# Kernel tuning notes

Hardware: AMD Instinct MI355X
Metric: run time of the kernel (lower is better)

## Reference

```python
import jax, jax.numpy as jnp
import numpy as np
import math

B, S, D = 4, 2048, 768
H = 12
DH = D // H  # 64
NEG = -1e10

def setup_inputs() -> dict:
    key = jax.random.key(0)
    ks = jax.random.split(key, 8)
    scale = 0.02
    return {
        "hidden_states": jax.random.normal(ks[0], (B, S, D), dtype=jnp.float32),
        "attention_mask": jnp.zeros((B, 1, 1, S), dtype=jnp.float32),
        "Wq": jax.random.normal(ks[1], (D, D), dtype=jnp.float32) * scale,
        "bq": jnp.zeros((D,), dtype=jnp.float32),
        "Wk": jax.random.normal(ks[2], (D, D), dtype=jnp.float32) * scale,
        "bk": jnp.zeros((D,), dtype=jnp.float32),
        "Wv": jax.random.normal(ks[3], (D, D), dtype=jnp.float32) * scale,
        "bv": jnp.zeros((D,), dtype=jnp.float32),
    }

def reference(hidden_states, attention_mask, Wq, bq, Wk, bk, Wv, bv):
    # Linear projections; note attention_mask is accepted but unused, matching the torch module.
    def split_heads(x):  # [B,S,D] -> [B,H,S,DH]
        return x.reshape(B, S, H, DH).transpose(0, 2, 1, 3)
    q = split_heads(hidden_states @ Wq + bq)
    k = split_heads(hidden_states @ Wk + bk)
    v = split_heads(hidden_states @ Wv + bv)
    scores = jnp.einsum("bhqd,bhkd->bhqk", q, k) / math.sqrt(DH)
    causal = jnp.tril(jnp.ones((S, S), dtype=bool))  # masked_fill(mask==0, -1e10)
    scores = jnp.where(causal, scores, NEG)
    probs = jax.nn.softmax(scores, axis=-1)
    # dropout prob = 0.0 (eval) -> identity
    ctx = jnp.einsum("bhqk,bhkd->bhqd", probs, v)
    return ctx.transpose(0, 2, 1, 3).reshape(B, S, D)
```

## Files before the change

kernel.cpp:

```cpp
#include <hip/hip_runtime.h>
#include <hip/hip_bf16.h>

#define B_  4
#define S_  2048
#define D_  768
#define H_  12
#define DH_ 64

#define QSCALE 0.1803368802f

typedef __bf16 bf16;
typedef __attribute__((ext_vector_type(8))) __bf16 bf16x8;
typedef __attribute__((ext_vector_type(4))) __bf16 bf16x4;
typedef __attribute__((ext_vector_type(4))) float floatx4;
typedef __attribute__((ext_vector_type(4))) short short4v;

#if defined(__has_builtin)
#if __has_builtin(__builtin_amdgcn_mfma_f32_16x16x16bf16_1k)
#define HAVE_MFMA16_BUILTIN 1
#endif
#endif
static __device__ __forceinline__ floatx4 mfma16(short4v a, short4v b, floatx4 c) {
#ifdef HAVE_MFMA16_BUILTIN
    return __builtin_amdgcn_mfma_f32_16x16x16bf16_1k(a, b, c, 0, 0, 0);
#else
    floatx4 d = c;
    asm("v_mfma_f32_16x16x16_bf16 %0, %1, %2, %0" : "+v"(d) : "v"(a), "v"(b));
    return d;
#endif
}

__device__ __forceinline__ int swz(int row, int col) {
    return row * 64 + (col ^ ((row & 7) << 3));
}

__device__ __forceinline__ void gload16(const bf16* g, bf16* l) {
    __builtin_amdgcn_global_load_lds(
        (const __attribute__((address_space(1))) void*)g,
        (__attribute__((address_space(3))) void*)l, 16, 0, 0);
}

__device__ __forceinline__ int chunk_off(int qt) {
    if (qt < 8)  return qt;
    if (qt < 16) return 8 + 2 * (qt - 8);
    if (qt < 24) return 24 + 3 * (qt - 16);
    return 48 + 4 * (qt - 24);
}

__global__ __launch_bounds__(256) void prep(const float* __restrict__ hs,
                                            const float* __restrict__ w0,
                                            const float* __restrict__ w1,
                                            const float* __restrict__ w2,
                                            bf16* __restrict__ Xb,
                                            bf16* __restrict__ Wt)
{
    __shared__ bf16 t[64 * 72];
    const int bid = blockIdx.x;
    const int tid = threadIdx.x;
    if (bid < 6144) {
        int i = bid * 256 + tid;
        float4 v = ((const float4*)hs)[i];
        bf16x4 o;
        o[0] = (bf16)v.x; o[1] = (bf16)v.y; o[2] = (bf16)v.z; o[3] = (bf16)v.w;
        *(bf16x4*)(Xb + (size_t)i * 4) = o;
        return;
    }
    const int t4 = bid - 6144;
    const int which = t4 / 144;
    const int rem = t4 % 144;
    const float* W = (which == 0) ? w0 : (which == 1 ? w1 : w2);
    const float sc = (which == 0) ? QSCALE : 1.0f;
    bf16* dst = Wt + (size_t)which * D_ * D_;
    const int k0 = (rem / 12) * 64, n0 = (rem % 12) * 64;
    {
        int r = tid >> 2;
        int c0 = (tid & 3) * 16;
        #pragma unroll
        for (int q = 0; q < 4; q++) {
            float4 v = *(const float4*)(W + (size_t)(k0 + r) * D_ + n0 + c0 + q * 4);
            t[(c0 + q * 4 + 0) * 72 + r] = (bf16)(v.x * sc);
            t[(c0 + q * 4 + 1) * 72 + r] = (bf16)(v.y * sc);
            t[(c0 + q * 4 + 2) * 72 + r] = (bf16)(v.z * sc);
            t[(c0 + q * 4 + 3) * 72 + r] = (bf16)(v.w * sc);
        }
    }
    __syncthreads();
    {
        int n = tid >> 3, seg = tid & 7;
        *(bf16x8*)(dst + (size_t)(n0 + n) * D_ + k0 + seg * 8) =
            *(const bf16x8*)(t + n * 72 + seg * 8);
        *(bf16x8*)(dst + (size_t)(n0 + n + 32) * D_ + k0 + seg * 8) =
            *(const bf16x8*)(t + (n + 32) * 72 + seg * 8);
    }
}

__global__ __launch_bounds__(256) void qkv_gemm(
    const bf16* __restrict__ Xb, const bf16* __restrict__ Wt,
    const float* __restrict__ bq, const float* __restrict__ bk,
    const float* __restrict__ bv, bf16* __restrict__ QKV)
{
    const int which = blockIdx.z;
    const bf16* Wm = Wt + (size_t)which * D_ * D_;
    const float* bias = (which == 0) ? bq : (which == 1 ? bk : bv);
    const float bscale = (which == 0) ? QSCALE : 1.0f;
    bf16* out = QKV + (size_t)which * B_ * H_ * S_ * DH_;

    __shared__ bf16 As[128 * 64];
    __shared__ bf16 Bs[128 * 64];

    const int tid  = threadIdx.x;
    const int wave = tid >> 6, lane = tid & 63;
    const int wr = wave >> 1, wc = wave & 1;
    const int g = lane >> 4, ln = lane & 15;
    const int m0 = blockIdx.x * 128, n0 = blockIdx.y * 128;

    floatx4 acc[4][4];
    #pragma unroll
    for (int i = 0; i < 4; i++)
        #pragma unroll
        for (int j = 0; j < 4; j++)
            acc[i][j] = (floatx4){0.f, 0.f, 0.f, 0.f};

    int row_[4], scol_[4];
    #pragma unroll
    for (int t = 0; t < 4; t++) {
        int c = tid + t * 256;
        row_[t]  = c >> 3;
        scol_[t] = ((c & 7) * 8) ^ ((row_[t] & 7) << 3);
    }

    for (int k0 = 0; k0 < D_; k0 += 64) {
        if (k0) __syncthreads();
        #pragma unroll
        for (int t = 0; t < 4; t++) {
            bf16* ldst = As + (size_t)(t * 256 + wave * 64) * 8;
            gload16(Xb + (size_t)(m0 + row_[t]) * D_ + k0 + scol_[t], ldst);
        }
        #pragma unroll
        for (int t = 0; t < 4; t++) {
            bf16* ldst = Bs + (size_t)(t * 256 + wave * 64) * 8;
            gload16(Wm + (size_t)(n0 + row_[t]) * D_ + k0 + scol_[t], ldst);
        }
        __syncthreads();
        #pragma unroll
        for (int ks = 0; ks < 2; ks++) {
            bf16x8 af[4], bfr[4];
            #pragma unroll
            for (int i = 0; i < 4; i++)
                af[i] = *(const bf16x8*)(As + swz(wr * 64 + i * 16 + ln, ks * 32 + g * 8));
            #pragma unroll
            for (int j = 0; j < 4; j++)
                bfr[j] = *(const bf16x8*)(Bs + swz(wc * 64 + j * 16 + ln, ks * 32 + g * 8));
            if (which == 2) {
                #pragma unroll
                for (int i = 0; i < 4; i++)
                    #pragma unroll
                    for (int j = 0; j < 4; j++)
                        acc[i][j] = __builtin_amdgcn_mfma_f32_16x16x32_bf16(af[i], bfr[j], acc[i][j], 0, 0, 0);
            } else {
                #pragma unroll
                for (int i = 0; i < 4; i++)
                    #pragma unroll
                    for (int j = 0; j < 4; j++)
                        acc[i][j] = __builtin_amdgcn_mfma_f32_16x16x32_bf16(bfr[j], af[i], acc[i][j], 0, 0, 0);
            }
        }
    }

    if (which == 2) {
        #pragma unroll
        for (int i = 0; i < 4; i++) {
            #pragma unroll
            for (int j = 0; j < 4; j++) {
                int col = n0 + wc * 64 + j * 16 + ln;
                float bv_ = bias[col];
                int h = col >> 6, dh = col & 63;
                int rowbase = m0 + wr * 64 + i * 16 + g * 4;
                int b = rowbase >> 11, s0 = rowbase & 2047;
                bf16x4 o;
                #pragma unroll
                for (int r = 0; r < 4; r++) o[r] = (bf16)(acc[i][j][r] + bv_);
                *(bf16x4*)(out + ((size_t)((b * H_ + h) * DH_ + dh)) * S_ + s0) = o;
            }
        }
    } else {
        #pragma unroll
        for (int i = 0; i < 4; i++) {
            int s = m0 + wr * 64 + i * 16 + ln;
            int b = s >> 11, s0 = s & 2047;
            #pragma unroll
            for (int j = 0; j < 4; j++) {
                int nb = n0 + wc * 64 + j * 16 + g * 4;
                int h = nb >> 6, dh0 = nb & 63;
                float4 bv4 = *(const float4*)(bias + nb);
                bf16x4 o;
                o[0] = (bf16)(acc[i][j][0] + bv4.x * bscale);
                o[1] = (bf16)(acc[i][j][1] + bv4.y * bscale);
                o[2] = (bf16)(acc[i][j][2] + bv4.z * bscale);
                o[3] = (bf16)(acc[i][j][3] + bv4.w * bscale);
                *(bf16x4*)(out + (((size_t)(b * H_ + h) * S_ + s0) << 6) + dh0) = o;
            }
        }
    }
}

__global__ __launch_bounds__(256, 4) void attn_chunk(const bf16* __restrict__ QKV,
                                                     float* __restrict__ out,
                                                     bf16* __restrict__ Opart,
                                                     float* __restrict__ Lpart)
{
    const int cid = 79 - blockIdx.x;
    const int bh = blockIdx.y;
    const int b = bh / H_, h = bh % H_;

    int qt, c;
    if (cid < 8)       { qt = cid; c = 0; }
    else if (cid < 24) { qt = 8 + ((cid - 8) >> 1); c = (cid - 8) & 1; }
    else if (cid < 48) { int t3 = cid - 24; qt = 16 + t3 / 3; c = t3 - (qt - 16) * 3; }
    else               { int t4 = cid - 48; qt = 24 + (t4 >> 2); c = t4 & 3; }
    const int nch = (qt >> 3) + 1;
    const int kt0 = c * 8;
    const int kt1 = min(kt0 + 7, qt);

    const size_t MAT = (size_t)B_ * H_ * S_ * DH_;
    const bf16* Q  = QKV +           (size_t)bh * S_ * DH_;
    const bf16* K  = QKV + MAT +     (size_t)bh * S_ * DH_;
    const bf16* Vt = QKV + 2 * MAT + (size_t)bh * S_ * DH_;

    __shared__ bf16 Ks[64 * 64];
    __shared__ bf16 Vts[64 * 64];

    const int tid  = threadIdx.x;
    const int wave = tid >> 6, lane = tid & 63;
    const int g = lane >> 4, ln = lane & 15;
    const int srow = tid >> 3, sseg = tid & 7;

    bf16x8 qf[2];
    {
        const bf16* qrow = Q + (size_t)(qt * 64 + wave * 16 + ln) * DH_;
        qf[0] = *(const bf16x8*)(qrow + g * 8);
        qf[1] = *(const bf16x8*)(qrow + 32 + g * 8);
    }

    const short4v ones16 = {0x3F80, 0x3F80, 0x3F80, 0x3F80};

    floatx4 accO[4];
    #pragma unroll
    for (int dt = 0; dt < 4; dt++) accO[dt] = (floatx4){0.f, 0.f, 0.f, 0.f};
    floatx4 accL = (floatx4){0.f, 0.f, 0.f, 0.f};

    const bf16* kptr = K  + (size_t)(kt0 * 64 + srow) * DH_ + sseg * 8;
    const bf16* vptr = Vt + (size_t)srow * S_ + kt0 * 64 + sseg * 8;

    bf16x8 ka = *(const bf16x8*)kptr;
    bf16x8 kb = *(const bf16x8*)(kptr + 32 * DH_);
    bf16x8 va = *(const bf16x8*)vptr;
    bf16x8 vb = *(const bf16x8*)(vptr + (size_t)32 * S_);

    for (int kt = kt0; kt <= kt1; ++kt) {
        __syncthreads();
        *(bf16x8*)(Ks  + swz(srow, sseg * 8)) = ka;
        *(bf16x8*)(Ks  + swz(srow + 32, sseg * 8)) = kb;
        *(bf16x8*)(Vts + swz(srow, sseg * 8)) = va;
        *(bf16x8*)(Vts + swz(srow + 32, sseg * 8)) = vb;
        __syncthreads();
        if (kt < kt1) {
            kptr += 64 * DH_;
            vptr += 64;
            ka = *(const bf16x8*)kptr;
            kb = *(const bf16x8*)(kptr + 32 * DH_);
            va = *(const bf16x8*)vptr;
            vb = *(const bf16x8*)(vptr + (size_t)32 * S_);
        }

        __builtin_amdgcn_s_setprio(1);
        #pragma unroll
        for (int j = 0; j < 4; j++) {
            floatx4 accS = (floatx4){0.f, 0.f, 0.f, 0.f};
            #pragma unroll
            for (int cc = 0; cc < 2; cc++) {
                bf16x8 kf = *(const bf16x8*)(Ks + swz(j * 16 + ln, cc * 32 + g * 8));
                accS = __builtin_amdgcn_mfma_f32_16x16x32_bf16(kf, qf[cc], accS, 0, 0, 0);
            }

            #pragma unroll
            for (int r = 0; r < 4; r++) accS[r] = __builtin_amdgcn_exp2f(accS[r]);
            if (kt == qt) {
                const int krow = j * 16 + g * 4;
                const int qrow = wave * 16 + ln;
                #pragma unroll
                for (int r = 0; r < 4; r++)
                    if (krow + r > qrow) accS[r] = 0.f;
            }

            bf16x4 pa;
            #pragma unroll
            for (int r = 0; r < 4; r++) pa[r] = (bf16)accS[r];
            short4v pas = __builtin_bit_cast(short4v, pa);

            accL = mfma16(pas, ones16, accL);

            #pragma unroll
            for (int dt = 0; dt < 4; dt++) {
                short4v vf = *(const short4v*)(Vts + swz(dt * 16 + ln, j * 16 + g * 4));
                accO[dt] = mfma16(pas, vf, accO[dt]);
            }
        }
        __builtin_amdgcn_s_setprio(0);
    }

    if (nch == 1) {
        float inv[4];
        #pragma unroll
        for (int r = 0; r < 4; r++) inv[r] = 1.0f / accL[r];
        #pragma unroll
        for (int dt = 0; dt < 4; dt++) {
            int dh = dt * 16 + ln;
            #pragma unroll
            for (int r = 0; r < 4; r++) {
                int q = qt * 64 + wave * 16 + g * 4 + r;
                out[((size_t)(b * S_ + q)) * D_ + h * DH_ + dh] = accO[dt][r] * inv[r];
            }
        }
    } else {
        const int chunk = bh * 80 + chunk_off(qt) + c;
        bf16x8 p0, p1;
        #pragma unroll
        for (int e = 0; e < 8; e++) {
            p0[e] = (bf16)accO[e >> 2][e & 3];
            p1[e] = (bf16)accO[2 + (e >> 2)][e & 3];
        }
        bf16* dst = Opart + (size_t)chunk * 4096 + tid * 16;
        *(bf16x8*)dst = p0;
        *(bf16x8*)(dst + 8) = p1;
        if (ln == 0) {
            #pragma unroll
            for (int r = 0; r < 4; r++)
                Lpart[chunk * 64 + wave * 16 + g * 4 + r] = accL[r];
        }
    }
}

__global__ __launch_bounds__(256) void attn_reduce(const bf16* __restrict__ Opart,
                                                   const float* __restrict__ Lpart,
                                                   float* __restrict__ out)
{
    const int qt = 8 + blockIdx.x;
    const int bh = blockIdx.y;
    const int b = bh / H_, h = bh % H_;
    const int nch = (qt >> 3) + 1;
    const int cb = bh * 80 + chunk_off(qt);

    const int tid  = threadIdx.x;
    const int wave = tid >> 6, lane = tid & 63;
    const int g = lane >> 4, ln = lane & 15;

    float o[16];
    #pragma unroll
    for (int e = 0; e < 16; e++) o[e] = 0.f;
    float ls[4] = {0.f, 0.f, 0.f, 0.f};

    for (int cidx = 0; cidx < nch; cidx++) {
        const bf16* p = Opart + (size_t)(cb + cidx) * 4096 + tid * 16;
        bf16x8 v0 = *(const bf16x8*)p;
        bf16x8 v1 = *(const bf16x8*)(p + 8);
        #pragma unroll
        for (int e = 0; e < 8; e++) { o[e] += (float)v0[e]; o[8 + e] += (float)v1[e]; }
        #pragma unroll
        for (int r = 0; r < 4; r++)
            ls[r] += Lpart[(cb + cidx) * 64 + wave * 16 + g * 4 + r];
    }
    float inv[4];
    #pragma unroll
    for (int r = 0; r < 4; r++) inv[r] = 1.0f / ls[r];
    #pragma unroll
    for (int j = 0; j < 4; j++) {
        int dh = j * 16 + ln;
        #pragma unroll
        for (int r = 0; r < 4; r++) {
            int q = qt * 64 + wave * 16 + g * 4 + r;
            out[((size_t)(b * S_ + q)) * D_ + h * DH_ + dh] = o[j * 4 + r] * inv[r];
        }
    }
}

extern "C" void kernel_launch(void* const* d_in, const int* in_sizes, int n_in,
                              void* d_out, int out_size, void* d_ws, size_t ws_size,
                              hipStream_t stream) {
    const float* hs = (const float*)d_in[0];
    const float* Wq = (const float*)d_in[2];
    const float* bq = (const float*)d_in[3];
    const float* Wk = (const float*)d_in[4];
    const float* bk = (const float*)d_in[5];
    const float* Wv = (const float*)d_in[6];
    const float* bv = (const float*)d_in[7];
    float* out = (float*)d_out;

    bf16* Xb    = (bf16*)d_ws;
    bf16* Wt    = Xb + (size_t)8192 * 768;
    bf16* QKV   = Wt + (size_t)3 * 768 * 768;
    bf16* Opart = QKV + (size_t)3 * B_ * H_ * S_ * DH_;
    float* Lpart = (float*)(Opart + (size_t)3840 * 4096);

    prep<<<6576, 256, 0, stream>>>(hs, Wq, Wk, Wv, Xb, Wt);
    qkv_gemm<<<dim3(64, 6, 3), 256, 0, stream>>>(Xb, Wt, bq, bk, bv, QKV);
    attn_chunk<<<dim3(80, 48), 256, 0, stream>>>(QKV, out, Opart, Lpart);
    attn_reduce<<<dim3(24, 48), 256, 0, stream>>>(Opart, Lpart, out);
}
```

Measured before the change: 220.4 us.

## Process two query tiles per attention block to reuse K/V tiles

Each attention_chunk block now handles two adjacent 64-row query tiles (128 queries), so every K/V tile staged in shared memory feeds twice as many MFMAs. The grid halves from 80 to 40 chunks per head, and the partial-output and row-sum buffers are relaid out to hold both tiles per chunk. The V-projection epilogue is also unified with the Q/K path: operand order is swapped and the transposed V is written as scalar strided stores. The cost is higher register pressure from the doubled accumulators, fewer blocks for load balancing, and less coalesced writes for V.

```diff
diff --git a/kernel.cpp b/kernel.cpp
--- a/kernel.cpp
+++ b/kernel.cpp
@@ -40,11 +40,11 @@
         (__attribute__((address_space(3))) void*)l, 16, 0, 0);
 }
 
-__device__ __forceinline__ int chunk_off(int qt) {
-    if (qt < 8)  return qt;
-    if (qt < 16) return 8 + 2 * (qt - 8);
-    if (qt < 24) return 24 + 3 * (qt - 16);
-    return 48 + 4 * (qt - 24);
+__device__ __forceinline__ int chunk_off(int qb) {
+    if (qb < 4)  return qb;
+    if (qb < 8)  return 4 + 2 * (qb - 4);
+    if (qb < 12) return 12 + 3 * (qb - 8);
+    return 24 + 4 * (qb - 12);
 }
 
 __global__ __launch_bounds__(256) void prep(const float* __restrict__ hs,
@@ -132,15 +132,13 @@
     for (int k0 = 0; k0 < D_; k0 += 64) {
         if (k0) __syncthreads();
         #pragma unroll
-        for (int t = 0; t < 4; t++) {
-            bf16* ldst = As + (size_t)(t * 256 + wave * 64) * 8;
-            gload16(Xb + (size_t)(m0 + row_[t]) * D_ + k0 + scol_[t], ldst);
-        }
-        #pragma unroll
-        for (int t = 0; t < 4; t++) {
-            bf16* ldst = Bs + (size_t)(t * 256 + wave * 64) * 8;
-            gload16(Wm + (size_t)(n0 + row_[t]) * D_ + k0 + scol_[t], ldst);
-        }
+        for (int t = 0; t < 4; t++)
+            gload16(Xb + (size_t)(m0 + row_[t]) * D_ + k0 + scol_[t],
+                    As + (size_t)(t * 256 + wave * 64) * 8);
+        #pragma unroll
+        for (int t = 0; t < 4; t++)
+            gload16(Wm + (size_t)(n0 + row_[t]) * D_ + k0 + scol_[t],
+                    Bs + (size_t)(t * 256 + wave * 64) * 8);
         __syncthreads();
         #pragma unroll
         for (int ks = 0; ks < 2; ks++) {
@@ -151,39 +149,15 @@
             #pragma unroll
             for (int j = 0; j < 4; j++)
                 bfr[j] = *(const bf16x8*)(Bs + swz(wc * 64 + j * 16 + ln, ks * 32 + g * 8));
-            if (which == 2) {
+            #pragma unroll
+            for (int i = 0; i < 4; i++)
                 #pragma unroll
-                for (int i = 0; i < 4; i++)
-                    #pragma unroll
-                    for (int j = 0; j < 4; j++)
-                        acc[i][j] = __builtin_amdgcn_mfma_f32_16x16x32_bf16(af[i], bfr[j], acc[i][j], 0, 0, 0);
-            } else {
-                #pragma unroll
-                for (int i = 0; i < 4; i++)
-                    #pragma unroll
-                    for (int j = 0; j < 4; j++)
-                        acc[i][j] = __builtin_amdgcn_mfma_f32_16x16x32_bf16(bfr[j], af[i], acc[i][j], 0, 0, 0);
-            }
-        }
-    }
-
-    if (which == 2) {
-        #pragma unroll
-        for (int i = 0; i < 4; i++) {
-            #pragma unroll
-            for (int j = 0; j < 4; j++) {
-                int col = n0 + wc * 64 + j * 16 + ln;
-                float bv_ = bias[col];
-                int h = col >> 6, dh = col & 63;
-                int rowbase = m0 + wr * 64 + i * 16 + g * 4;
-                int b = rowbase >> 11, s0 = rowbase & 2047;
-                bf16x4 o;
-                #pragma unroll
-                for (int r = 0; r < 4; r++) o[r] = (bf16)(acc[i][j][r] + bv_);
-                *(bf16x4*)(out + ((size_t)((b * H_ + h) * DH_ + dh)) * S_ + s0) = o;
-            }
-        }
-    } else {
+                for (int j = 0; j < 4; j++)
+                    acc[i][j] = __builtin_amdgcn_mfma_f32_16x16x32_bf16(bfr[j], af[i], acc[i][j], 0, 0, 0);
+        }
+    }
+
+    if (which < 2) {
         #pragma unroll
         for (int i = 0; i < 4; i++) {
             int s = m0 + wr * 64 + i * 16 + ln;
@@ -201,6 +175,23 @@
                 *(bf16x4*)(out + (((size_t)(b * H_ + h) * S_ + s0) << 6) + dh0) = o;
             }
         }
+    } else {
+        #pragma unroll
+        for (int i = 0; i < 4; i++) {
+            int s = m0 + wr * 64 + i * 16 + ln;
+            int b = s >> 11, s0 = s & 2047;
+            #pragma unroll
+            for (int j = 0; j < 4; j++) {
+                int nb = n0 + wc * 64 + j * 16 + g * 4;
+                int h = nb >> 6, dh0 = nb & 63;
+                float4 bv4 = *(const float4*)(bias + nb);
+                bf16* base = out + ((size_t)(b * H_ + h) * DH_ + dh0) * S_ + s0;
+                base[0]          = (bf16)(acc[i][j][0] + bv4.x);
+                base[S_]         = (bf16)(acc[i][j][1] + bv4.y);
+                base[2 * S_]     = (bf16)(acc[i][j][2] + bv4.z);
+                base[3 * (size_t)S_] = (bf16)(acc[i][j][3] + bv4.w);
+            }
+        }
     }
 }
 
@@ -209,18 +200,19 @@
                                                      bf16* __restrict__ Opart,
                                                      float* __restrict__ Lpart)
 {
-    const int cid = 79 - blockIdx.x;
+    const int cid = 39 - blockIdx.x;
     const int bh = blockIdx.y;
     const int b = bh / H_, h = bh % H_;
 
-    int qt, c;
-    if (cid < 8)       { qt = cid; c = 0; }
-    else if (cid < 24) { qt = 8 + ((cid - 8) >> 1); c = (cid - 8) & 1; }
-    else if (cid < 48) { int t3 = cid - 24; qt = 16 + t3 / 3; c = t3 - (qt - 16) * 3; }
-    else               { int t4 = cid - 48; qt = 24 + (t4 >> 2); c = t4 & 3; }
-    const int nch = (qt >> 3) + 1;
+    int qb, c;
+    if (cid < 4)       { qb = cid; c = 0; }
+    else if (cid < 12) { qb = 4 + ((cid - 4) >> 1); c = (cid - 4) & 1; }
+    else if (cid < 24) { int t = cid - 12; qb = 8 + t / 3; c = t - (qb - 8) * 3; }
+    else               { int t = cid - 24; qb = 12 + (t >> 2); c = t & 3; }
+    const int nch = (qb >> 2) + 1;
+    const int qt0 = 2 * qb, qt1 = 2 * qb + 1;
     const int kt0 = c * 8;
-    const int kt1 = min(kt0 + 7, qt);
+    const int kt1 = min(kt0 + 7, qt1);
 
     const size_t MAT = (size_t)B_ * H_ * S_ * DH_;
     const bf16* Q  = QKV +           (size_t)bh * S_ * DH_;
@@ -235,19 +227,26 @@
     const int g = lane >> 4, ln = lane & 15;
     const int srow = tid >> 3, sseg = tid & 7;
 
-    bf16x8 qf[2];
+    bf16x8 qf0[2], qf1[2];
     {
-        const bf16* qrow = Q + (size_t)(qt * 64 + wave * 16 + ln) * DH_;
-        qf[0] = *(const bf16x8*)(qrow + g * 8);
-        qf[1] = *(const bf16x8*)(qrow + 32 + g * 8);
+        const bf16* qrow = Q + (size_t)(qt0 * 64 + wave * 16 + ln) * DH_;
+        qf0[0] = *(const bf16x8*)(qrow + g * 8);
+        qf0[1] = *(const bf16x8*)(qrow + 32 + g * 8);
+        qrow += (size_t)64 * DH_;
+        qf1[0] = *(const bf16x8*)(qrow + g * 8);
+        qf1[1] = *(const bf16x8*)(qrow + 32 + g * 8);
     }
 
     const short4v ones16 = {0x3F80, 0x3F80, 0x3F80, 0x3F80};
 
-    floatx4 accO[4];
-    #pragma unroll
-    for (int dt = 0; dt < 4; dt++) accO[dt] = (floatx4){0.f, 0.f, 0.f, 0.f};
-    floatx4 accL = (floatx4){0.f, 0.f, 0.f, 0.f};
+    floatx4 accO0[4], accO1[4];
+    #pragma unroll
+    for (int dt = 0; dt < 4; dt++) {
+        accO0[dt] = (floatx4){0.f, 0.f, 0.f, 0.f};
+        accO1[dt] = (floatx4){0.f, 0.f, 0.f, 0.f};
+    }
+    floatx4 accL0 = (floatx4){0.f, 0.f, 0.f, 0.f};
+    floatx4 accL1 = (floatx4){0.f, 0.f, 0.f, 0.f};
 
     const bf16* kptr = K  + (size_t)(kt0 * 64 + srow) * DH_ + sseg * 8;
     const bf16* vptr = Vt + (size_t)srow * S_ + kt0 * 64 + sseg * 8;
@@ -273,70 +272,98 @@
             vb = *(const bf16x8*)(vptr + (size_t)32 * S_);
         }
 
+        const bool do0 = (kt <= qt0);
+
         __builtin_amdgcn_s_setprio(1);
         #pragma unroll
         for (int j = 0; j < 4; j++) {
-            floatx4 accS = (floatx4){0.f, 0.f, 0.f, 0.f};
-            #pragma unroll
-            for (int cc = 0; cc < 2; cc++) {
-                bf16x8 kf = *(const bf16x8*)(Ks + swz(j * 16 + ln, cc * 32 + g * 8));
-                accS = __builtin_amdgcn_mfma_f32_16x16x32_bf16(kf, qf[cc], accS, 0, 0, 0);
-            }
-
-            #pragma unroll
-            for (int r = 0; r < 4; r++) accS[r] = __builtin_amdgcn_exp2f(accS[r]);
-            if (kt == qt) {
-                const int krow = j * 16 + g * 4;
-                const int qrow = wave * 16 + ln;
+            bf16x8 kfa = *(const bf16x8*)(Ks + swz(j * 16 + ln, g * 8));
+            bf16x8 kfb = *(const bf16x8*)(Ks + swz(j * 16 + ln, 32 + g * 8));
+
+            floatx4 accS0 = (floatx4){0.f, 0.f, 0.f, 0.f};
+            floatx4 accS1 = (floatx4){0.f, 0.f, 0.f, 0.f};
+            if (do0) {
+                accS0 = __builtin_amdgcn_mfma_f32_16x16x32_bf16(kfa, qf0[0], accS0, 0, 0, 0);
+                accS0 = __builtin_amdgcn_mfma_f32_16x16x32_bf16(kfb, qf0[1], accS0, 0, 0, 0);
+            }
+            accS1 = __builtin_amdgcn_mfma_f32_16x16x32_bf16(kfa, qf1[0], accS1, 0, 0, 0);
+            accS1 = __builtin_amdgcn_mfma_f32_16x16x32_bf16(kfb, qf1[1], accS1, 0, 0, 0);
+
+            const int krow = j * 16 + g * 4;
+            const int qrow = wave * 16 + ln;
+            #pragma unroll
+            for (int r = 0; r < 4; r++) {
+                accS0[r] = __builtin_amdgcn_exp2f(accS0[r]);
+                accS1[r] = __builtin_amdgcn_exp2f(accS1[r]);
+            }
+            if (kt == qt0) {
                 #pragma unroll
                 for (int r = 0; r < 4; r++)
-                    if (krow + r > qrow) accS[r] = 0.f;
-            }
-
-            bf16x4 pa;
-            #pragma unroll
-            for (int r = 0; r < 4; r++) pa[r] = (bf16)accS[r];
-            short4v pas = __builtin_bit_cast(short4v, pa);
-
-            accL = mfma16(pas, ones16, accL);
+                    if (krow + r > qrow) accS0[r] = 0.f;
+            }
+            if (kt == qt1) {
+                #pragma unroll
+                for (int r = 0; r < 4; r++)
+                    if (krow + r > qrow) accS1[r] = 0.f;
+            }
+
+            bf16x4 pa0, pa1;
+            #pragma unroll
+            for (int r = 0; r < 4; r++) { pa0[r] = (bf16)accS0[r]; pa1[r] = (bf16)accS1[r]; }
+            short4v pas0 = __builtin_bit_cast(short4v, pa0);
+            short4v pas1 = __builtin_bit_cast(short4v, pa1);
+
+            if (do0) accL0 = mfma16(pas0, ones16, accL0);
+            accL1 = mfma16(pas1, ones16, accL1);
 
             #pragma unroll
             for (int dt = 0; dt < 4; dt++) {
                 short4v vf = *(const short4v*)(Vts + swz(dt * 16 + ln, j * 16 + g * 4));
-                accO[dt] = mfma16(pas, vf, accO[dt]);
+                if (do0) accO0[dt] = mfma16(pas0, vf, accO0[dt]);
+                accO1[dt] = mfma16(pas1, vf, accO1[dt]);
             }
         }
         __builtin_amdgcn_s_setprio(0);
     }
 
     if (nch == 1) {
-        float inv[4];
-        #pragma unroll
-        for (int r = 0; r < 4; r++) inv[r] = 1.0f / accL[r];
+        float inv0[4], inv1[4];
+        #pragma unroll
+        for (int r = 0; r < 4; r++) { inv0[r] = 1.0f / accL0[r]; inv1[r] = 1.0f / accL1[r]; }
         #pragma unroll
         for (int dt = 0; dt < 4; dt++) {
             int dh = dt * 16 + ln;
             #pragma unroll
             for (int r = 0; r < 4; r++) {
-                int q = qt * 64 + wave * 16 + g * 4 + r;
-                out[((size_t)(b * S_ + q)) * D_ + h * DH_ + dh] = accO[dt][r] * inv[r];
+                int q0 = qt0 * 64 + wave * 16 + g * 4 + r;
+                out[((size_t)(b * S_ + q0)) * D_ + h * DH_ + dh] = accO0[dt][r] * inv0[r];
+                out[((size_t)(b * S_ + q0 + 64)) * D_ + h * DH_ + dh] = accO1[dt][r] * inv1[r];
             }
         }
     } else {
-        const int chunk = bh * 80 + chunk_off(qt) + c;
+        const int chunk = bh * 40 + chunk_off(qb) + c;
+        bf16* dst = Opart + (size_t)chunk * 8192 + tid * 16;
         bf16x8 p0, p1;
         #pragma unroll
         for (int e = 0; e < 8; e++) {
-            p0[e] = (bf16)accO[e >> 2][e & 3];
-            p1[e] = (bf16)accO[2 + (e >> 2)][e & 3];
-        }
-        bf16* dst = Opart + (size_t)chunk * 4096 + tid * 16;
+            p0[e] = (bf16)accO0[e >> 2][e & 3];
+            p1[e] = (bf16)accO0[2 + (e >> 2)][e & 3];
+        }
         *(bf16x8*)dst = p0;
         *(bf16x8*)(dst + 8) = p1;
+        #pragma unroll
+        for (int e = 0; e < 8; e++) {
+            p0[e] = (bf16)accO1[e >> 2][e & 3];
+            p1[e] = (bf16)accO1[2 + (e >> 2)][e & 3];
+        }
+        *(bf16x8*)(dst + 4096) = p0;
+        *(bf16x8*)(dst + 4104) = p1;
         if (ln == 0) {
             #pragma unroll
-            for (int r = 0; r < 4; r++)
-                Lpart[chunk * 64 + wave * 16 + g * 4 + r] = accL[r];
+            for (int r = 0; r < 4; r++) {
+                Lpart[chunk * 128 + wave * 16 + g * 4 + r] = accL0[r];
+                Lpart[chunk * 128 + 64 + wave * 16 + g * 4 + r] = accL1[r];
+            }
         }
     }
 }
@@ -346,10 +373,11 @@
                                                    float* __restrict__ out)
 {
     const int qt = 8 + blockIdx.x;
+    const int qb = qt >> 1, sub = qt & 1;
     const int bh = blockIdx.y;
     const int b = bh / H_, h = bh % H_;
-    const int nch = (qt >> 3) + 1;
-    const int cb = bh * 80 + chunk_off(qt);
+    const int nch = (qb >> 2) + 1;
+    const int cb = bh * 40 + chunk_off(qb);
 
     const int tid  = threadIdx.x;
     const int wave = tid >> 6, lane = tid & 63;
@@ -361,14 +389,14 @@
     float ls[4] = {0.f, 0.f, 0.f, 0.f};
 
     for (int cidx = 0; cidx < nch; cidx++) {
-        const bf16* p = Opart + (size_t)(cb + cidx) * 4096 + tid * 16;
+        const bf16* p = Opart + (size_t)(cb + cidx) * 8192 + sub * 4096 + tid * 16;
         bf16x8 v0 = *(const bf16x8*)p;
         bf16x8 v1 = *(const bf16x8*)(p + 8);
         #pragma unroll
         for (int e = 0; e < 8; e++) { o[e] += (float)v0[e]; o[8 + e] += (float)v1[e]; }
         #pragma unroll
         for (int r = 0; r < 4; r++)
-            ls[r] += Lpart[(cb + cidx) * 64 + wave * 16 + g * 4 + r];
+            ls[r] += Lpart[(cb + cidx) * 128 + sub * 64 + wave * 16 + g * 4 + r];
     }
     float inv[4];
     #pragma unroll
@@ -400,10 +428,10 @@
     bf16* Wt    = Xb + (size_t)8192 * 768;
     bf16* QKV   = Wt + (size_t)3 * 768 * 768;
     bf16* Opart = QKV + (size_t)3 * B_ * H_ * S_ * DH_;
-    float* Lpart = (float*)(Opart + (size_t)3840 * 4096);
+    float* Lpart = (float*)(Opart + (size_t)1920 * 8192);
 
     prep<<<6576, 256, 0, stream>>>(hs, Wq, Wk, Wv, Xb, Wt);
     qkv_gemm<<<dim3(64, 6, 3), 256, 0, stream>>>(Xb, Wt, bq, bk, bv, QKV);
-    attn_chunk<<<dim3(80, 48), 256, 0, stream>>>(QKV, out, Opart, Lpart);
+    attn_chunk<<<dim3(40, 48), 256, 0, stream>>>(QKV, out, Opart, Lpart);
     attn_reduce<<<dim3(24, 48), 256, 0, stream>>>(Opart, Lpart, out);
 }
```

Result: slower. 407.9 us (+85.1%).
